# Performance work log

Hardware: AMD Instinct MI355X
Metric: run time of the kernel (lower is better)

## Reference

```python
import jax, jax.numpy as jnp
import numpy as np

VOCAB = 40
BATCH = 262144
SEQLEN = 128


def setup_inputs() -> dict:
    key = jax.random.key(0)
    x = jax.random.randint(key, (BATCH, SEQLEN), 0, VOCAB, dtype=jnp.int32)
    return {"x": x}


def reference(x) -> jnp.ndarray:
    # x: [B, L] int token ids; 0 is padding (excluded from stats).
    B = x.shape[0]
    valid = (x != 0).astype(jnp.float32)  # [B, L]
    # Per-row histogram via scatter-add; pad positions scatter 0.0 into bin 0.
    rows = jnp.arange(B, dtype=jnp.int32)[:, None]
    counts = jnp.zeros((B, VOCAB), jnp.float32).at[rows, x].add(valid)  # [B, V]
    total = counts.sum(axis=-1, keepdims=True)  # [B, 1]
    nonempty = total[:, 0] > 0  # [B]
    probs = counts / jnp.maximum(total, 1.0)  # [B, V]
    pos = counts > 0
    unique = pos.sum(axis=-1).astype(jnp.float32) / VOCAB  # unique_chars / vocab
    max_freq = probs.max(axis=-1)
    min_freq = jnp.where(pos, probs, jnp.inf).min(axis=-1)
    min_freq = jnp.where(nonempty, min_freq, 0.0)
    letter_ratio = probs[:, 1:27].sum(axis=-1)
    digit_ratio = probs[:, 27:37].sum(axis=-1)
    special_ratio = probs[:, 37:].sum(axis=-1)
    feats = jnp.stack(
        [unique, max_freq, min_freq, letter_ratio, digit_ratio, special_ratio],
        axis=-1,
    )  # [B, 6]
    # Rows with no valid (nonzero) tokens produce all-zero features.
    return jnp.where(nonempty[:, None], feats, 0.0)
```

## Files before the change

kernel.cpp:

```cpp
#include <hip/hip_runtime.h>

#define VOCAB 40
#define SEQ 128
#define THREADS 256
#define ROWS_PB 32
#define NW 10


__global__ __launch_bounds__(THREADS) void char_dist_kernel(
    const int* __restrict__ x, float* __restrict__ out, int batch) {
  __shared__ unsigned int hist[NW * THREADS];
  const int tid = threadIdx.x;
  const int l = tid & 7;
  const int gb = tid & ~7;
  const int row = blockIdx.x * ROWS_PB + (tid >> 3);
  const bool active = row < batch;

  unsigned int* hb = &hist[tid];
#pragma unroll
  for (int w = 0; w < NW; ++w) hb[w * THREADS] = 0u;

  if (active) {
    const int4* gp = reinterpret_cast<const int4*>(x) + ((long)row << 5) + l;
    const int4 t0 = gp[0];
    const int4 t1 = gp[8];
    const int4 t2 = gp[16];
    const int4 t3 = gp[24];
#define HADD(t) hb[(((unsigned)(t)) >> 2) * THREADS] += 1u << (((t) & 3) << 3);
    HADD(t0.x) HADD(t0.y) HADD(t0.z) HADD(t0.w)
    HADD(t1.x) HADD(t1.y) HADD(t1.z) HADD(t1.w)
    HADD(t2.x) HADD(t2.y) HADD(t2.z) HADD(t2.w)
    HADD(t3.x) HADD(t3.y) HADD(t3.z) HADD(t3.w)
  }
  __builtin_amdgcn_wave_barrier();

  int total = 0, uniq = 0, maxc = 0, minc = 0x7fffffff;
  int letters = 0, digits = 0;

  {
    unsigned int m = 0;
#pragma unroll
    for (int j = 0; j < 8; ++j)
      m += hist[l * THREADS + gb + ((j + l) & 7)];
    const int bin0 = l * 4;
#pragma unroll
    for (int b = 0; b < 4; ++b) {
      const int bin = bin0 + b;
      int c = (int)((m >> (b * 8)) & 0xFFu);
      c = (bin == 0) ? 0 : c;
      total += c;
      uniq += (c > 0) ? 1 : 0;
      maxc = max(maxc, c);
      minc = (c > 0) ? min(minc, c) : minc;
      letters += (bin <= 26) ? c : 0;
      digits += (bin >= 27 && bin <= 36) ? c : 0;
    }
  }
  if (l < 2) {
    const int w = l + 8;
    unsigned int m = 0;
#pragma unroll
    for (int j = 0; j < 8; ++j)
      m += hist[w * THREADS + gb + ((j + l) & 7)];
    const int bin0 = w * 4;
#pragma unroll
    for (int b = 0; b < 4; ++b) {
      const int bin = bin0 + b;
      const int c = (int)((m >> (b * 8)) & 0xFFu);
      total += c;
      uniq += (c > 0) ? 1 : 0;
      maxc = max(maxc, c);
      minc = (c > 0) ? min(minc, c) : minc;
      digits += (bin <= 36) ? c : 0;
    }
  }

  unsigned int S = (unsigned)total | ((unsigned)letters << 10) |
                   ((unsigned)digits << 20);
#pragma unroll
  for (int d = 1; d < 8; d <<= 1) {
    S += __shfl_xor(S, d);
    uniq += __shfl_xor(uniq, d);
    maxc = max(maxc, __shfl_xor(maxc, d));
    minc = min(minc, __shfl_xor(minc, d));
  }

  if (active && l == 0) {
    const int totalR = (int)(S & 0x3FFu);
    const int lettersR = (int)((S >> 10) & 0x3FFu);
    const int digitsR = (int)((S >> 20) & 0x3FFu);
    const int specialR = totalR - lettersR - digitsR;
    float f0, f1, f2, f3, f4, f5;
    if (totalR > 0) {
      const float inv = 1.0f / (float)totalR;
      f0 = (float)uniq * (1.0f / (float)VOCAB);
      f1 = (float)maxc * inv;
      f2 = (float)minc * inv;
      f3 = (float)lettersR * inv;
      f4 = (float)digitsR * inv;
      f5 = (float)specialR * inv;
    } else {
      f0 = f1 = f2 = f3 = f4 = f5 = 0.0f;
    }
    float2* o = reinterpret_cast<float2*>(out + (long)row * 6);
    o[0] = make_float2(f0, f1);
    o[1] = make_float2(f2, f3);
    o[2] = make_float2(f4, f5);
  }
}

extern "C" void kernel_launch(void* const* d_in, const int* in_sizes, int n_in,
                              void* d_out, int out_size, void* d_ws, size_t ws_size,
                              hipStream_t stream) {
  const int* x = (const int*)d_in[0];
  float* out = (float*)d_out;
  const int batch = in_sizes[0] / SEQ;
  const int blocks = (batch + ROWS_PB - 1) / ROWS_PB;
  char_dist_kernel<<<blocks, THREADS, 0, stream>>>(x, out, batch);
}
```

Baseline: 186.2 us.

## Replace per-thread packed histograms with shared per-row LDS atomic histogram

Each group of 8 threads now builds one 40-bin histogram per row in shared memory with LDS atomicAdd, using a padded stride of 41. This replaces ten private packed-byte counters per thread that needed serial read-modify-write chains and an 8-way merge. Each thread then reads its 5 bins directly, and the unique count is packed into the shuffled sum word, which drops one shuffle reduction chain. The trade is atomic contention when several lanes hit the same bin, in exchange for less LDS use (which may raise occupancy) and a shorter reduction.

```diff
diff --git a/kernel.cpp b/kernel.cpp
--- a/kernel.cpp
+++ b/kernel.cpp
@@ -4,21 +4,23 @@
 #define SEQ 128
 #define THREADS 256
 #define ROWS_PB 32
-#define NW 10
+#define GSTRIDE 41
 
 
 __global__ __launch_bounds__(THREADS) void char_dist_kernel(
     const int* __restrict__ x, float* __restrict__ out, int batch) {
-  __shared__ unsigned int hist[NW * THREADS];
+  __shared__ unsigned int hist[ROWS_PB * GSTRIDE];
   const int tid = threadIdx.x;
   const int l = tid & 7;
-  const int gb = tid & ~7;
-  const int row = blockIdx.x * ROWS_PB + (tid >> 3);
+  const int g = tid >> 3;
+  const int row = blockIdx.x * ROWS_PB + g;
   const bool active = row < batch;
 
-  unsigned int* hb = &hist[tid];
+  unsigned int* gh = &hist[g * GSTRIDE];
+  const int b0 = 5 * l;
 #pragma unroll
-  for (int w = 0; w < NW; ++w) hb[w * THREADS] = 0u;
+  for (int j = 0; j < 5; ++j) gh[b0 + j] = 0u;
+  __builtin_amdgcn_wave_barrier();
 
   if (active) {
     const int4* gp = reinterpret_cast<const int4*>(x) + ((long)row << 5) + l;
@@ -26,7 +28,7 @@
     const int4 t1 = gp[8];
     const int4 t2 = gp[16];
     const int4 t3 = gp[24];
-#define HADD(t) hb[(((unsigned)(t)) >> 2) * THREADS] += 1u << (((t) & 3) << 3);
+#define HADD(t) atomicAdd(&gh[(t)], 1u);
     HADD(t0.x) HADD(t0.y) HADD(t0.z) HADD(t0.w)
     HADD(t1.x) HADD(t1.y) HADD(t1.z) HADD(t1.w)
     HADD(t2.x) HADD(t2.y) HADD(t2.z) HADD(t2.w)
@@ -34,66 +36,46 @@
   }
   __builtin_amdgcn_wave_barrier();
 
-  int total = 0, uniq = 0, maxc = 0, minc = 0x7fffffff;
-  int letters = 0, digits = 0;
+  int c0 = (int)gh[b0 + 0];
+  int c1 = (int)gh[b0 + 1];
+  int c2 = (int)gh[b0 + 2];
+  int c3 = (int)gh[b0 + 3];
+  int c4 = (int)gh[b0 + 4];
+  if (l == 0) c0 = 0;
 
-  {
-    unsigned int m = 0;
-#pragma unroll
-    for (int j = 0; j < 8; ++j)
-      m += hist[l * THREADS + gb + ((j + l) & 7)];
-    const int bin0 = l * 4;
-#pragma unroll
-    for (int b = 0; b < 4; ++b) {
-      const int bin = bin0 + b;
-      int c = (int)((m >> (b * 8)) & 0xFFu);
-      c = (bin == 0) ? 0 : c;
-      total += c;
-      uniq += (c > 0) ? 1 : 0;
-      maxc = max(maxc, c);
-      minc = (c > 0) ? min(minc, c) : minc;
-      letters += (bin <= 26) ? c : 0;
-      digits += (bin >= 27 && bin <= 36) ? c : 0;
-    }
+  int total = 0, uniq = 0, maxc = 0, minc = 255, letters = 0, digits = 0;
+#define STAT(j, cc)                                                          \
+  {                                                                          \
+    const int bin = b0 + (j);                                                \
+    total += (cc);                                                           \
+    uniq += ((cc) > 0) ? 1 : 0;                                              \
+    maxc = max(maxc, (cc));                                                  \
+    minc = min(minc, ((cc) > 0) ? (cc) : 255);                               \
+    letters += (bin <= 26) ? (cc) : 0;                                       \
+    digits += (bin >= 27 && bin <= 36) ? (cc) : 0;                           \
   }
-  if (l < 2) {
-    const int w = l + 8;
-    unsigned int m = 0;
-#pragma unroll
-    for (int j = 0; j < 8; ++j)
-      m += hist[w * THREADS + gb + ((j + l) & 7)];
-    const int bin0 = w * 4;
-#pragma unroll
-    for (int b = 0; b < 4; ++b) {
-      const int bin = bin0 + b;
-      const int c = (int)((m >> (b * 8)) & 0xFFu);
-      total += c;
-      uniq += (c > 0) ? 1 : 0;
-      maxc = max(maxc, c);
-      minc = (c > 0) ? min(minc, c) : minc;
-      digits += (bin <= 36) ? c : 0;
-    }
-  }
+  STAT(0, c0) STAT(1, c1) STAT(2, c2) STAT(3, c3) STAT(4, c4)
+#undef STAT
 
-  unsigned int S = (unsigned)total | ((unsigned)letters << 10) |
-                   ((unsigned)digits << 20);
+  unsigned int S = (unsigned)total | ((unsigned)letters << 8) |
+                   ((unsigned)digits << 16) | ((unsigned)uniq << 24);
 #pragma unroll
   for (int d = 1; d < 8; d <<= 1) {
     S += __shfl_xor(S, d);
-    uniq += __shfl_xor(uniq, d);
     maxc = max(maxc, __shfl_xor(maxc, d));
     minc = min(minc, __shfl_xor(minc, d));
   }
 
   if (active && l == 0) {
-    const int totalR = (int)(S & 0x3FFu);
-    const int lettersR = (int)((S >> 10) & 0x3FFu);
-    const int digitsR = (int)((S >> 20) & 0x3FFu);
+    const int totalR = (int)(S & 0xFFu);
+    const int lettersR = (int)((S >> 8) & 0xFFu);
+    const int digitsR = (int)((S >> 16) & 0xFFu);
+    const int uniqR = (int)(S >> 24);
     const int specialR = totalR - lettersR - digitsR;
     float f0, f1, f2, f3, f4, f5;
     if (totalR > 0) {
       const float inv = 1.0f / (float)totalR;
-      f0 = (float)uniq * (1.0f / (float)VOCAB);
+      f0 = (float)uniqR * (1.0f / (float)VOCAB);
       f1 = (float)maxc * inv;
       f2 = (float)minc * inv;
       f3 = (float)lettersR * inv;
```

Result: no change. 186.0 us (-0.1%).
